# Performance work log

Measured on AMD Instinct MI355X. Metric: run time of the kernel, lower is better.

## Reference

```python
import jax, jax.numpy as jnp
import numpy as np

N, H, C, K = 8192, 1024, 1024, 32  # tokens, nhid, ncls, words-per-class (vocab = C*K = 32768)
R = 0.1  # init_weights uniform range


def setup_inputs() -> dict:
    key = jax.random.key(0)
    k0, k1, k2, k3 = jax.random.split(key, 4)
    x = jax.random.normal(k0, (N, H), jnp.float32)
    cls = jax.random.randint(k1, (N,), 0, C)  # per-token class id (derived from word2cls[target])
    W_cls = jax.random.uniform(k2, (C, H), jnp.float32, -R, R)
    b_cls = jnp.zeros((C,), jnp.float32)
    W_words = jax.random.uniform(k3, (C, K, H), jnp.float32, -R, R)  # stacked per-class Linear weights
    b_words = jnp.zeros((C, K), jnp.float32)
    return {"x": x, "cls": cls, "W_cls": W_cls, "b_cls": b_cls,
            "W_words": W_words, "b_words": b_words}


def reference(x, cls, W_cls, b_cls, W_words, b_words):
    # Class head: nn.Linear(nhid, ncls) over all tokens -> [N, C]
    p_class = x @ W_cls.T + b_cls
    # Per-class word heads: original gathers tokens per class (index_select) and
    # applies that class's nn.Linear(nhid, K). Equivalent grouped form: gather each
    # token's class weights and do a batched matvec. p_words[i] are the within-class
    # logits of token i under class cls[i] (same math, token order instead of
    # dict-of-classes order).
    Wg = W_words[cls]                                   # [N, K, H]
    p_words = jnp.einsum('nh,nkh->nk', x, Wg) + b_words[cls]  # [N, K]
    return p_class, p_words
```

## Files before the change

kernel.cpp:

```cpp
#include <hip/hip_runtime.h>
#include <stdint.h>

#define HDIM 1024
#define CDIM 1024
#define KW   32
#define CAP  64

typedef unsigned short u16;
typedef __attribute__((ext_vector_type(8))) short bf16x8;
typedef __attribute__((ext_vector_type(4))) float f32x4;

#define GLDS16(gp, lp)                                                                    \
  __builtin_amdgcn_global_load_lds((const __attribute__((address_space(1))) void*)(gp),   \
                                   (__attribute__((address_space(3))) void*)(lp), 16, 0, 0)

__device__ __forceinline__ u16 f2bf(float f) {
  union { float f; unsigned u; } v; v.f = f;
  unsigned r = v.u + 0x7FFFu + ((v.u >> 16) & 1u);
  return (u16)(r >> 16);
}

__device__ __forceinline__ bf16x8 pack8(float4 a, float4 b) {
  bf16x8 r;
  r[0] = (short)f2bf(a.x); r[1] = (short)f2bf(a.y);
  r[2] = (short)f2bf(a.z); r[3] = (short)f2bf(a.w);
  r[4] = (short)f2bf(b.x); r[5] = (short)f2bf(b.y);
  r[6] = (short)f2bf(b.z); r[7] = (short)f2bf(b.w);
  return r;
}

__global__ __launch_bounds__(256) void convert_and_zero(const float* __restrict__ x,
                                                        u16* __restrict__ xbf, int n4x,
                                                        const float* __restrict__ Wc,
                                                        u16* __restrict__ wbf, int n4w,
                                                        int* __restrict__ cursor) {
  const int tid0 = blockIdx.x * 256 + threadIdx.x;
  if (tid0 < CDIM) cursor[tid0] = 0;
  const int total = n4x + n4w;
  const int stride = gridDim.x * 256;
  for (int j = tid0; j < total; j += stride) {
    float4 v;
    if (j < n4x) v = ((const float4*)x)[j];
    else         v = ((const float4*)Wc)[j - n4x];
    ushort4 o;
    o.x = f2bf(v.x); o.y = f2bf(v.y); o.z = f2bf(v.z); o.w = f2bf(v.w);
    if (j < n4x) ((ushort4*)xbf)[j] = o;
    else         ((ushort4*)wbf)[j - n4x] = o;
  }
}

__global__ __launch_bounds__(256) void scatter_kernel(const int* __restrict__ cls, int N,
                                                      int* __restrict__ cursor,
                                                      int* __restrict__ toklist) {
  const int i = blockIdx.x * 256 + threadIdx.x;
  if (i < N) {
    const int c = cls[i];
    const int pos = atomicAdd(&cursor[c], 1);
    if (pos < CAP) toklist[c * CAP + pos] = i;
  }
}

#define GEMM_STAGE(BUF, KT)                                       \
  GLDS16(xb + ga0 + (KT), As + (BUF) * 4096 + (size_t)c0 * 8);    \
  GLDS16(xb + ga1 + (KT), As + (BUF) * 4096 + (size_t)c1 * 8);    \
  GLDS16(wb + gb0 + (KT), Bs + (BUF) * 4096 + (size_t)c0 * 8);    \
  GLDS16(wb + gb1 + (KT), Bs + (BUF) * 4096 + (size_t)c1 * 8);

#define GEMM_COMPUTE(BUF)                                                                    \
  {                                                                                          \
    bf16x8 a[4], b[4];                                                                       \
    _Pragma("unroll") for (int m = 0; m < 4; m++)                                            \
      a[m] = *(const bf16x8*)&As[(BUF) * 4096 + (wr * 64 + m * 16 + fr) * 32 + koff];        \
    _Pragma("unroll") for (int n = 0; n < 4; n++)                                            \
      b[n] = *(const bf16x8*)&Bs[(BUF) * 4096 + (wc * 64 + n * 16 + fr) * 32 + koff];        \
    _Pragma("unroll") for (int m = 0; m < 4; m++)                                            \
      _Pragma("unroll") for (int n = 0; n < 4; n++)                                          \
        acc[m][n] = __builtin_amdgcn_mfma_f32_16x16x32_bf16(a[m], b[n], acc[m][n], 0, 0, 0); \
  }

__device__ __forceinline__ void gemm_block(int gid, char* smem,
                                           const u16* __restrict__ xb,
                                           const u16* __restrict__ wb,
                                           const float* __restrict__ bcls,
                                           float* __restrict__ out) {
  u16* As = (u16*)smem;
  u16* Bs = (u16*)smem + 8192;
  const int tid  = threadIdx.x;
  const int lane = tid & 63;
  const int wid  = tid >> 6;
  const int wr   = wid >> 1, wc = wid & 1;
  const int bm = gid >> 3, bn = gid & 7;

  const int c0 = tid, c1 = tid + 256;
  const size_t ga0 = (size_t)(bm * 128 + (c0 >> 2)) * HDIM + (c0 & 3) * 8;
  const size_t ga1 = (size_t)(bm * 128 + (c1 >> 2)) * HDIM + (c1 & 3) * 8;
  const size_t gb0 = (size_t)(bn * 128 + (c0 >> 2)) * HDIM + (c0 & 3) * 8;
  const size_t gb1 = (size_t)(bn * 128 + (c1 >> 2)) * HDIM + (c1 & 3) * 8;

  f32x4 acc[4][4] = {};

  const int fr   = lane & 15;
  const int koff = (lane >> 4) * 8;

  GEMM_STAGE(0, 0);
  __syncthreads();
  int cur = 0;
#pragma unroll 2
  for (int kt = 0; kt < HDIM - 32; kt += 32) {
    GEMM_STAGE(cur ^ 1, kt + 32);
    GEMM_COMPUTE(cur);
    __syncthreads();
    cur ^= 1;
  }
  GEMM_COMPUTE(cur);

  const int crow = (lane >> 4) * 4;
  const int ccol = lane & 15;
#pragma unroll
  for (int n = 0; n < 4; n++) {
    const int col   = bn * 128 + wc * 64 + n * 16 + ccol;
    const float bias = bcls[col];
#pragma unroll
    for (int m = 0; m < 4; m++) {
      const int row0 = bm * 128 + wr * 64 + m * 16 + crow;
#pragma unroll
      for (int r = 0; r < 4; r++)
        out[(size_t)(row0 + r) * CDIM + col] = acc[m][n][r] + bias;
    }
  }
}

__device__ __forceinline__ void words_block(int c, char* smem,
                                            const u16* __restrict__ xbf,
                                            const float* __restrict__ Ww,
                                            const float* __restrict__ bw,
                                            const int* __restrict__ toklist,
                                            const int* __restrict__ cursor,
                                            float* __restrict__ outw) {
  const int count = min(cursor[c], CAP);
  if (count <= 0) return;
  float* red = (float*)smem;
  int* toks  = (int*)(smem + 8192);
  const int tid  = threadIdx.x;
  const int lane = tid & 63, wave = tid >> 6;
  const int fr   = lane & 15;
  const int koff = (lane >> 4) * 8;
  const float* Wc = Ww + (size_t)c * KW * HDIM;
  const int k0 = wave * 256;

  for (int base = 0; base < count; base += 16) {
    const int nt = min(16, count - base);
    __syncthreads();
    if (tid < 16) toks[tid] = toklist[c * CAP + base + min(tid, nt - 1)];
    __syncthreads();
    const u16* arow = xbf + (size_t)toks[fr] * HDIM;
    const float* b0row = Wc + (size_t)fr * HDIM;
    const float* b1row = Wc + (size_t)(16 + fr) * HDIM;
    f32x4 acc0 = {}, acc1 = {};
#pragma unroll
    for (int ks = 0; ks < 8; ks++) {
      const int kt = k0 + ks * 32 + koff;
      bf16x8 a = *(const bf16x8*)(arow + kt);
      float4 b0a = *(const float4*)(b0row + kt);
      float4 b0b = *(const float4*)(b0row + kt + 4);
      float4 b1a = *(const float4*)(b1row + kt);
      float4 b1b = *(const float4*)(b1row + kt + 4);
      bf16x8 b0 = pack8(b0a, b0b);
      bf16x8 b1 = pack8(b1a, b1b);
      acc0 = __builtin_amdgcn_mfma_f32_16x16x32_bf16(a, b0, acc0, 0, 0, 0);
      acc1 = __builtin_amdgcn_mfma_f32_16x16x32_bf16(a, b1, acc1, 0, 0, 0);
    }
    const int rb = (lane >> 4) * 4, cc = lane & 15;
#pragma unroll
    for (int r = 0; r < 4; r++) {
      red[((wave * 2 + 0) * 16 + rb + r) * 16 + cc] = acc0[r];
      red[((wave * 2 + 1) * 16 + rb + r) * 16 + cc] = acc1[r];
    }
    __syncthreads();
    const int row = tid >> 4, col = tid & 15;
#pragma unroll
    for (int wcx = 0; wcx < 2; wcx++) {
      float s = 0.f;
#pragma unroll
      for (int w = 0; w < 4; w++) s += red[((w * 2 + wcx) * 16 + row) * 16 + col];
      if (row < nt) {
        const int word = wcx * 16 + col;
        outw[(size_t)toks[row] * KW + word] = s + bw[c * KW + word];
      }
    }
  }
}

__global__ __launch_bounds__(256) void mega_kernel(const u16* __restrict__ xbf,
                                                   const u16* __restrict__ wbf,
                                                   const float* __restrict__ bc,
                                                   float* __restrict__ out,
                                                   const float* __restrict__ Ww,
                                                   const float* __restrict__ bw,
                                                   const int* __restrict__ toklist,
                                                   const int* __restrict__ cursor,
                                                   float* __restrict__ outw, int nbg) {
  __shared__ __align__(16) char smem[32832];
  const int bid = blockIdx.x;
  if (2 * nbg == CDIM) {
    if (bid % 3 == 0) gemm_block(bid / 3, smem, xbf, wbf, bc, out);
    else              words_block(bid - bid / 3 - 1, smem, xbf, Ww, bw, toklist, cursor, outw);
  } else {
    if (bid < nbg) gemm_block(bid, smem, xbf, wbf, bc, out);
    else           words_block(bid - nbg, smem, xbf, Ww, bw, toklist, cursor, outw);
  }
}

__global__ __launch_bounds__(256) void words_kernel(const float* __restrict__ x,
                                                    const int* __restrict__ cls,
                                                    const float* __restrict__ Ww,
                                                    const float* __restrict__ bw,
                                                    float* __restrict__ outw) {
  const int n    = blockIdx.x;
  const int c    = cls[n];
  const int lane = threadIdx.x & 63;
  const int wave = threadIdx.x >> 6;
  const float4* xr = (const float4*)(x + (size_t)n * HDIM);
  float4 xv[4];
#pragma unroll
  for (int i = 0; i < 4; i++) xv[i] = xr[lane + 64 * i];
  const float* Wc = Ww + (size_t)c * KW * HDIM;
#pragma unroll
  for (int wi = 0; wi < 8; wi++) {
    const int w = wave * 8 + wi;
    const float4* wrp = (const float4*)(Wc + (size_t)w * HDIM);
    float s = 0.f;
#pragma unroll
    for (int i = 0; i < 4; i++) {
      float4 wv = wrp[lane + 64 * i];
      s += xv[i].x * wv.x + xv[i].y * wv.y + xv[i].z * wv.z + xv[i].w * wv.w;
    }
#pragma unroll
    for (int off = 32; off > 0; off >>= 1) s += __shfl_down(s, off);
    if (lane == 0) outw[(size_t)n * KW + w] = s + bw[c * KW + w];
  }
}

__global__ __launch_bounds__(256) void gemm_f32_naive(const float* __restrict__ x,
                                                      const float* __restrict__ Wc,
                                                      const float* __restrict__ bc,
                                                      float* __restrict__ out) {
  __shared__ float xs[HDIM];
  const int n = blockIdx.x;
  const int tid = threadIdx.x;
  ((float4*)xs)[tid] = ((const float4*)(x + (size_t)n * HDIM))[tid];
  __syncthreads();
  for (int c = tid; c < CDIM; c += 256) {
    const float* wr = Wc + (size_t)c * HDIM;
    float s = 0.f;
    for (int h = 0; h < HDIM; h += 4) {
      float4 wv = *(const float4*)(wr + h);
      s += xs[h] * wv.x + xs[h + 1] * wv.y + xs[h + 2] * wv.z + xs[h + 3] * wv.w;
    }
    out[(size_t)n * CDIM + c] = s + bc[c];
  }
}

extern "C" void kernel_launch(void* const* d_in, const int* in_sizes, int n_in,
                              void* d_out, int out_size, void* d_ws, size_t ws_size,
                              hipStream_t stream) {
  const float* x   = (const float*)d_in[0];
  const int*   cls = (const int*)d_in[1];
  const float* Wc  = (const float*)d_in[2];
  const float* bc  = (const float*)d_in[3];
  const float* Ww  = (const float*)d_in[4];
  const float* bw  = (const float*)d_in[5];
  float* out = (float*)d_out;
  const int N = in_sizes[0] / HDIM;
  float* outw = out + (size_t)N * CDIM;

  const size_t bf_bytes  = ((size_t)N * HDIM + (size_t)CDIM * HDIM) * sizeof(u16);
  const size_t ints_off  = (bf_bytes + 63) & ~(size_t)63;
  const size_t need_all  = ints_off + ((size_t)CDIM + (size_t)CDIM * CAP) * sizeof(int);

  if (ws_size >= need_all && (N % 128) == 0) {
    u16* xbf = (u16*)d_ws;
    u16* wbf = xbf + (size_t)N * HDIM;
    int* cursor  = (int*)((char*)d_ws + ints_off);
    int* toklist = cursor + CDIM;

    convert_and_zero<<<2048, 256, 0, stream>>>(x, xbf, N * HDIM / 4,
                                               Wc, wbf, CDIM * HDIM / 4, cursor);
    scatter_kernel<<<(N + 255) / 256, 256, 0, stream>>>(cls, N, cursor, toklist);
    const int nbg = (N / 128) * (CDIM / 128);
    mega_kernel<<<nbg + CDIM, 256, 0, stream>>>(xbf, wbf, bc, out, Ww, bw,
                                                toklist, cursor, outw, nbg);
  } else {
    gemm_f32_naive<<<N, 256, 0, stream>>>(x, Wc, bc, out);
    words_kernel<<<N, 256, 0, stream>>>(x, cls, Ww, bw, outw);
  }
}
```

Before: 72.05 us.

## Triple-buffer GEMM LDS pipeline with explicit vmcnt waits and priority hints

Reworks the class-head GEMM main loop from double-buffered LDS staging with __syncthreads to a three-stage ring, using explicit s_waitcnt vmcnt counts so two tiles of global->LDS loads stay in flight while the current one is consumed. It also hoists the bias loads before the loop and raises wave priority around the MFMA block. The aim is to hide global load latency better. In exchange LDS per block grows from about 32KB to 48KB, which can reduce occupancy for the mega kernel, and it relies on hand-counted vmcnt values being correct.

```diff
diff --git a/kernel.cpp b/kernel.cpp
--- a/kernel.cpp
+++ b/kernel.cpp
@@ -13,6 +13,8 @@
 #define GLDS16(gp, lp)                                                                    \
   __builtin_amdgcn_global_load_lds((const __attribute__((address_space(1))) void*)(gp),   \
                                    (__attribute__((address_space(3))) void*)(lp), 16, 0, 0)
+
+#define WAITV(N) asm volatile("s_waitcnt vmcnt(" #N ")" ::: "memory")
 
 __device__ __forceinline__ u16 f2bf(float f) {
   union { float f; unsigned u; } v; v.f = f;
@@ -60,19 +62,19 @@
   }
 }
 
-#define GEMM_STAGE(BUF, KT)                                       \
-  GLDS16(xb + ga0 + (KT), As + (BUF) * 4096 + (size_t)c0 * 8);    \
-  GLDS16(xb + ga1 + (KT), As + (BUF) * 4096 + (size_t)c1 * 8);    \
-  GLDS16(wb + gb0 + (KT), Bs + (BUF) * 4096 + (size_t)c0 * 8);    \
-  GLDS16(wb + gb1 + (KT), Bs + (BUF) * 4096 + (size_t)c1 * 8);
-
-#define GEMM_COMPUTE(BUF)                                                                    \
+#define STAGE_P(PA, PB, KT)                    \
+  GLDS16(xb + ga0 + (KT), (PA) + c0 * 8);      \
+  GLDS16(xb + ga1 + (KT), (PA) + c1 * 8);      \
+  GLDS16(wb + gb0 + (KT), (PB) + c0 * 8);      \
+  GLDS16(wb + gb1 + (KT), (PB) + c1 * 8);
+
+#define COMPUTE_P(PA, PB)                                                                    \
   {                                                                                          \
     bf16x8 a[4], b[4];                                                                       \
     _Pragma("unroll") for (int m = 0; m < 4; m++)                                            \
-      a[m] = *(const bf16x8*)&As[(BUF) * 4096 + (wr * 64 + m * 16 + fr) * 32 + koff];        \
+      a[m] = *(const bf16x8*)&(PA)[(wr * 64 + m * 16 + fr) * 32 + koff];                     \
     _Pragma("unroll") for (int n = 0; n < 4; n++)                                            \
-      b[n] = *(const bf16x8*)&Bs[(BUF) * 4096 + (wc * 64 + n * 16 + fr) * 32 + koff];        \
+      b[n] = *(const bf16x8*)&(PB)[(wc * 64 + n * 16 + fr) * 32 + koff];                     \
     _Pragma("unroll") for (int m = 0; m < 4; m++)                                            \
       _Pragma("unroll") for (int n = 0; n < 4; n++)                                          \
         acc[m][n] = __builtin_amdgcn_mfma_f32_16x16x32_bf16(a[m], b[n], acc[m][n], 0, 0, 0); \
@@ -84,7 +86,7 @@
                                            const float* __restrict__ bcls,
                                            float* __restrict__ out) {
   u16* As = (u16*)smem;
-  u16* Bs = (u16*)smem + 8192;
+  u16* Bs = (u16*)smem + 3 * 4096;
   const int tid  = threadIdx.x;
   const int lane = tid & 63;
   const int wid  = tid >> 6;
@@ -98,34 +100,51 @@
   const size_t gb1 = (size_t)(bn * 128 + (c1 >> 2)) * HDIM + (c1 & 3) * 8;
 
   f32x4 acc[4][4] = {};
-
   const int fr   = lane & 15;
   const int koff = (lane >> 4) * 8;
 
-  GEMM_STAGE(0, 0);
-  __syncthreads();
-  int cur = 0;
-#pragma unroll 2
-  for (int kt = 0; kt < HDIM - 32; kt += 32) {
-    GEMM_STAGE(cur ^ 1, kt + 32);
-    GEMM_COMPUTE(cur);
-    __syncthreads();
-    cur ^= 1;
-  }
-  GEMM_COMPUTE(cur);
+  const int ccol = lane & 15;
+  float bias[4];
+#pragma unroll
+  for (int n = 0; n < 4; n++) bias[n] = bcls[bn * 128 + wc * 64 + n * 16 + ccol];
+  WAITV(0);
+
+  u16 *A0 = As, *A1 = As + 4096, *A2 = As + 8192;
+  u16 *B0 = Bs, *B1 = Bs + 4096, *B2 = Bs + 8192;
+  STAGE_P(A0, B0, 0);
+  STAGE_P(A1, B1, 32);
+
+  for (int kt = 0; kt < HDIM; kt += 32) {
+    if (kt + 64 < HDIM) {
+      STAGE_P(A2, B2, kt + 64);
+      WAITV(8);
+    } else if (kt + 32 < HDIM) {
+      WAITV(4);
+    } else {
+      WAITV(0);
+    }
+    __builtin_amdgcn_s_barrier();
+    __builtin_amdgcn_sched_barrier(0);
+    __builtin_amdgcn_s_setprio(1);
+    COMPUTE_P(A0, B0);
+    __builtin_amdgcn_s_setprio(0);
+    __builtin_amdgcn_sched_barrier(0);
+    __builtin_amdgcn_s_barrier();
+    u16* t;
+    t = A0; A0 = A1; A1 = A2; A2 = t;
+    t = B0; B0 = B1; B1 = B2; B2 = t;
+  }
 
   const int crow = (lane >> 4) * 4;
-  const int ccol = lane & 15;
 #pragma unroll
   for (int n = 0; n < 4; n++) {
-    const int col   = bn * 128 + wc * 64 + n * 16 + ccol;
-    const float bias = bcls[col];
+    const int col = bn * 128 + wc * 64 + n * 16 + ccol;
 #pragma unroll
     for (int m = 0; m < 4; m++) {
       const int row0 = bm * 128 + wr * 64 + m * 16 + crow;
 #pragma unroll
       for (int r = 0; r < 4; r++)
-        out[(size_t)(row0 + r) * CDIM + col] = acc[m][n][r] + bias;
+        out[(size_t)(row0 + r) * CDIM + col] = acc[m][n][r] + bias[n];
     }
   }
 }
@@ -200,7 +219,7 @@
                                                    const int* __restrict__ toklist,
                                                    const int* __restrict__ cursor,
                                                    float* __restrict__ outw, int nbg) {
-  __shared__ __align__(16) char smem[32832];
+  __shared__ __align__(16) char smem[49216];
   const int bid = blockIdx.x;
   if (2 * nbg == CDIM) {
     if (bid % 3 == 0) gemm_block(bid / 3, smem, xbf, wbf, bc, out);
```

Result: slower. 75.38 us (+4.6%).
